# Optimization experiments

Measured on AMD Instinct MI355X. Metric: run time of the kernel, lower is better.

The kernel has to match this reference:

```python
import jax, jax.numpy as jnp
import numpy as np


def lstm_cell(x, h, c, Wih, Whh, bih, bhh):
    # PyTorch LSTMCell: gates ordered [i, f, g, o]
    gates = x @ Wih.T + h @ Whh.T + bih + bhh
    i, f, g, o = jnp.split(gates, 4, axis=-1)
    i = jax.nn.sigmoid(i)
    f = jax.nn.sigmoid(f)
    g = jnp.tanh(g)
    o = jax.nn.sigmoid(o)
    c_new = f * c + i * g
    h_new = o * jnp.tanh(c_new)
    return h_new, c_new


def setup_inputs() -> dict:
    key = jax.random.key(0)
    ks = jax.random.split(key, 16)
    B, T_ENC, T_CENT = 131072, 20, 100
    s32 = 1.0 / np.sqrt(32.0)
    s64 = 1.0 / np.sqrt(64.0)
    s96 = 1.0 / np.sqrt(96.0)
    f32 = jnp.float32
    return {
        "input_traj": jax.random.normal(ks[0], (B, T_ENC, 2), dtype=f32),
        "centerlines": jax.random.normal(ks[1], (B, T_CENT, 2), dtype=f32),
        "Wih_c": jax.random.normal(ks[2], (128, 2), dtype=f32) * s32,
        "Whh_c": jax.random.normal(ks[3], (128, 32), dtype=f32) * s32,
        "bih_c": jax.random.normal(ks[4], (128,), dtype=f32) * s32,
        "bhh_c": jax.random.normal(ks[5], (128,), dtype=f32) * s32,
        "Wih_e": jax.random.normal(ks[6], (256, 2), dtype=f32) * s64,
        "Whh_e": jax.random.normal(ks[7], (256, 64), dtype=f32) * s64,
        "bih_e": jax.random.normal(ks[8], (256,), dtype=f32) * s64,
        "bhh_e": jax.random.normal(ks[9], (256,), dtype=f32) * s64,
        "Wih_d": jax.random.normal(ks[10], (384, 96), dtype=f32) * s96,
        "Whh_d": jax.random.normal(ks[11], (384, 96), dtype=f32) * s96,
        "bih_d": jax.random.normal(ks[12], (384,), dtype=f32) * s96,
        "bhh_d": jax.random.normal(ks[13], (384,), dtype=f32) * s96,
        "W_emb": jax.random.normal(ks[14], (2, 96), dtype=f32) * s96,
        "b_emb": jax.random.normal(ks[15], (2,), dtype=f32) * s96,
    }


def reference(input_traj, centerlines, Wih_c, Whh_c, bih_c, bhh_c,
              Wih_e, Whh_e, bih_e, bhh_e, Wih_d, Whh_d, bih_d, bhh_d,
              W_emb, b_emb):
    B = input_traj.shape[0]
    DEC_STEPS = 30

    # --- centerline embedding LSTM (hidden 32) over max_len steps ---
    def cent_step(carry, x_t):
        h, c = carry
        h, c = lstm_cell(x_t, h, c, Wih_c, Whh_c, bih_c, bhh_c)
        return (h, c), None

    cent_init = (jnp.zeros((B, 32), input_traj.dtype), jnp.zeros((B, 32), input_traj.dtype))
    (cent_h, cent_c), _ = jax.lax.scan(cent_step, cent_init, jnp.swapaxes(centerlines, 0, 1))

    # --- encoder LSTM (hidden 64) over 20 steps ---
    def enc_step(carry, x_t):
        h, c = carry
        h, c = lstm_cell(x_t, h, c, Wih_e, Whh_e, bih_e, bhh_e)
        return (h, c), None

    enc_init = (jnp.zeros((B, 64), input_traj.dtype), jnp.zeros((B, 64), input_traj.dtype))
    (enc_h, enc_c), _ = jax.lax.scan(enc_step, enc_init, jnp.swapaxes(input_traj, 0, 1))

    # --- concat to 96-d state, decode 30 steps feeding h back as input ---
    h0 = jnp.concatenate([enc_h, cent_h], axis=1)  # [B, 96]
    c0 = jnp.concatenate([enc_c, cent_c], axis=1)

    def dec_step(carry, _):
        h, c = carry
        h, c = lstm_cell(h, h, c, Wih_d, Whh_d, bih_d, bhh_d)
        pos = h @ W_emb.T + b_emb  # [B, 2]
        return (h, c), pos

    (_, _), outs = jax.lax.scan(dec_step, (h0, c0), None, length=DEC_STEPS)
    pred_traj = jnp.swapaxes(outs, 0, 1)  # [B, 30, 2]
    return pred_traj
```

## Files before the change

kernel.cpp:

```cpp
#include <hip/hip_runtime.h>


#define B_TOTAL 131072
#define TB 48
#define NBLK ((B_TOTAL + TB - 1) / TB)

typedef __attribute__((ext_vector_type(8))) short bf16x8;
typedef __attribute__((ext_vector_type(4))) float f32x4;

#define MFMA16(a, b, c) __builtin_amdgcn_mfma_f32_16x16x32_bf16((a), (b), (c), 0, 0, 0)

#ifndef __has_builtin
#define __has_builtin(x) 0
#endif
#if __has_builtin(__builtin_amdgcn_exp2f)
#define EXP2(x) __builtin_amdgcn_exp2f(x)
#else
#define EXP2(x) exp2f(x)
#endif
#if __has_builtin(__builtin_amdgcn_rcpf)
#define RCPF(x) __builtin_amdgcn_rcpf(x)
#else
#define RCPF(x) (1.0f / (x))
#endif

#define L2E 1.44269504088896340736f
#define NEG2L2E (-2.88539008177792681472f)

#define OFF_WD_HI 0
#define OFF_WD_LO 36864
#define OFF_WE_HI 73728
#define OFF_WE_LO 98304
#define OFF_WC_HI 122880
#define OFF_WC_LO 131072
#define OFF_WM_HI 139264
#define OFF_WM_LO 140800
#define OFF_BIAS  142336

__device__ __forceinline__ void split2(float f, unsigned short& hi, unsigned short& lo)
{
  unsigned int u = __float_as_uint(f);
  hi = (unsigned short)(u >> 16);
  float r = f - __uint_as_float(u & 0xFFFF0000u);
  lo = (unsigned short)(__float_as_uint(r) >> 16);
}

__device__ __forceinline__ bf16x8 zero8()
{
  bf16x8 z;
#pragma unroll
  for (int e = 0; e < 8; ++e) z[e] = 0;
  return z;
}

__device__ __forceinline__ f32x4 splat4(float v)
{
  f32x4 a; a[0] = v; a[1] = v; a[2] = v; a[3] = v; return a;
}

__device__ __forceinline__ void load_x2(const float* __restrict__ base, long s, int stridef,
                                        int t, bool active, bf16x8& xhi, bf16x8& xlo)
{
  xhi = zero8(); xlo = zero8();
  if (active) {
    const float* p = base + s * (long)stridef + t * 2;
    float x0 = p[0], x1 = p[1];
    unsigned short h0, l0, h1, l1;
    split2(x0, h0, l0); split2(x1, h1, l1);
    xhi[0] = (short)h0; xhi[1] = (short)h1;
    xlo[0] = (short)l0; xlo[1] = (short)l1;
  }
}

__global__ void prep_weights(
    const float* __restrict__ Wih_c, const float* __restrict__ Whh_c,
    const float* __restrict__ bih_c, const float* __restrict__ bhh_c,
    const float* __restrict__ Wih_e, const float* __restrict__ Whh_e,
    const float* __restrict__ bih_e, const float* __restrict__ bhh_e,
    const float* __restrict__ Wih_d, const float* __restrict__ Whh_d,
    const float* __restrict__ bih_d, const float* __restrict__ bhh_d,
    const float* __restrict__ W_emb, const float* __restrict__ b_emb,
    unsigned short* __restrict__ wsu)
{
  int idx = blockIdx.x * 256 + threadIdx.x;
  float* wsf = (float*)(wsu + OFF_BIAS);
  unsigned short h, l;
  if (idx < 384 * 96) {
    int j = idx / 96;
    float s = (j >= 192 && j < 288) ? 2.0f * L2E : L2E;
    float w = (Wih_d[idx] + Whh_d[idx]) * s;
    split2(w, h, l);
    wsu[OFF_WD_HI + idx] = h; wsu[OFF_WD_LO + idx] = l;
  }
  if (idx < 256 * 96) {
    int j = idx / 96, k = idx - j * 96;
    float s = (j >= 128 && j < 192) ? 2.0f * L2E : L2E;
    float w = 0.0f;
    if (k < 64) w = Whh_e[j * 64 + k] * s;
    else if (k < 66) w = Wih_e[j * 2 + (k - 64)] * s;
    split2(w, h, l);
    wsu[OFF_WE_HI + idx] = h; wsu[OFF_WE_LO + idx] = l;
  }
  if (idx < 128 * 64) {
    int j = idx / 64, k = idx - j * 64;
    float s = (j >= 64 && j < 96) ? 2.0f * L2E : L2E;
    float w = 0.0f;
    if (k < 32) w = Whh_c[j * 32 + k] * s;
    else if (k < 34) w = Wih_c[j * 2 + (k - 32)] * s;
    split2(w, h, l);
    wsu[OFF_WC_HI + idx] = h; wsu[OFF_WC_LO + idx] = l;
  }
  if (idx < 16 * 96) {
    int n = idx / 96, k = idx - n * 96;
    float w = (n < 2) ? W_emb[n * 96 + k] : 0.0f;
    split2(w, h, l);
    wsu[OFF_WM_HI + idx] = h; wsu[OFF_WM_LO + idx] = l;
  }
  if (idx < 384) {
    float s = (idx >= 192 && idx < 288) ? 2.0f * L2E : L2E;
    wsf[idx] = (bih_d[idx] + bhh_d[idx]) * s;
  }
  if (idx < 256) {
    float s = (idx >= 128 && idx < 192) ? 2.0f * L2E : L2E;
    wsf[384 + idx] = (bih_e[idx] + bhh_e[idx]) * s;
  }
  if (idx < 128) {
    float s = (idx >= 64 && idx < 96) ? 2.0f * L2E : L2E;
    wsf[640 + idx] = (bih_c[idx] + bhh_c[idx]) * s;
  }
  if (idx < 2) wsf[768 + idx] = b_emb[idx];
}

__global__ __launch_bounds__(384, 2) void lstm_fused(
    const float* __restrict__ traj,
    const float* __restrict__ ctr,
    const unsigned short* __restrict__ wsu,
    float* __restrict__ out)
{
  const int tid = threadIdx.x;
  const int wid = tid >> 6;
  const int lane = tid & 63;
  const int lr = lane & 15;
  const int lg = lane >> 4;
  const int blk = blockIdx.x;

  const float* bias_d = (const float*)(wsu + OFF_BIAS);
  const float* bias_e = bias_d + 384;
  const float* bias_c = bias_d + 640;
  const float* bias_m = bias_d + 768;

  __shared__ __align__(16) unsigned short sh_hi[TB * 104];
  __shared__ __align__(16) unsigned short sh_lo[TB * 104];
  __shared__ __align__(16) unsigned short sBlo[384 * 104];
  __shared__ float sc[TB * 97];

  {
    unsigned int* p0 = (unsigned int*)sh_hi;
    unsigned int* p1 = (unsigned int*)sh_lo;
    for (int i = tid; i < TB * 104 / 2; i += 384) { p0[i] = 0u; p1[i] = 0u; }
  }
  __syncthreads();

  {
    const int ut = wid & 1;
    const int rg = wid >> 1;
    const int ucol = ut * 16 + lr;
    bf16x8 Bh_hi[4], Bh_lo[4], Bx_hi[4], Bx_lo[4];
    float bias[4];
#pragma unroll
    for (int g = 0; g < 4; ++g) {
      int j = g * 32 + ucol;
      Bh_hi[g] = *(const bf16x8*)(wsu + OFF_WC_HI + j * 64 + lg * 8);
      Bh_lo[g] = *(const bf16x8*)(wsu + OFF_WC_LO + j * 64 + lg * 8);
      Bx_hi[g] = *(const bf16x8*)(wsu + OFF_WC_HI + j * 64 + 32 + lg * 8);
      Bx_lo[g] = *(const bf16x8*)(wsu + OFF_WC_LO + j * 64 + 32 + lg * 8);
      bias[g] = bias_c[j];
    }
    float cr[4];
#pragma unroll
    for (int q = 0; q < 4; ++q) cr[q] = 0.0f;
    long srow = (long)blk * TB + rg * 16 + lr;
    if (srow > B_TOTAL - 1) srow = B_TOTAL - 1;
    bf16x8 Ah_hi = *(const bf16x8*)&sh_hi[(rg * 16 + lr) * 104 + 64 + lg * 8];
    bf16x8 Ah_lo = *(const bf16x8*)&sh_lo[(rg * 16 + lr) * 104 + 64 + lg * 8];
    bf16x8 Ax_hi, Ax_lo;
    load_x2(ctr, srow, 200, 0, lg == 0, Ax_hi, Ax_lo);
    for (int t = 0; t < 100; ++t) {
      f32x4 acc[4];
#pragma unroll
      for (int g = 0; g < 4; ++g) {
        f32x4 a = splat4(bias[g]);
        a = MFMA16(Ah_hi, Bh_hi[g], a);
        a = MFMA16(Ah_lo, Bh_hi[g], a);
        a = MFMA16(Ah_hi, Bh_lo[g], a);
        a = MFMA16(Ax_hi, Bx_hi[g], a);
        a = MFMA16(Ax_lo, Bx_hi[g], a);
        a = MFMA16(Ax_hi, Bx_lo[g], a);
        acc[g] = a;
      }
      __syncthreads();
#pragma unroll
      for (int q = 0; q < 4; ++q) {
        float ig = acc[0][q], fg = acc[1][q], gg = acc[2][q], og = acc[3][q];
        float si = RCPF(1.0f + EXP2(-ig));
        float sf = RCPF(1.0f + EXP2(-fg));
        float so = RCPF(1.0f + EXP2(-og));
        float tg = 2.0f * RCPF(1.0f + EXP2(-gg)) - 1.0f;
        float cn = sf * cr[q] + si * tg;
        cr[q] = cn;
        float tc = 2.0f * RCPF(1.0f + EXP2(cn * NEG2L2E)) - 1.0f;
        float hv = so * tc;
        unsigned short hh, hl;
        split2(hv, hh, hl);
        int r = rg * 16 + lg * 4 + q;
        sh_hi[r * 104 + 64 + ucol] = hh;
        sh_lo[r * 104 + 64 + ucol] = hl;
      }
      __syncthreads();
      Ah_hi = *(const bf16x8*)&sh_hi[(rg * 16 + lr) * 104 + 64 + lg * 8];
      Ah_lo = *(const bf16x8*)&sh_lo[(rg * 16 + lr) * 104 + 64 + lg * 8];
      int tn = t < 99 ? t + 1 : 99;
      load_x2(ctr, srow, 200, tn, lg == 0, Ax_hi, Ax_lo);
    }
#pragma unroll
    for (int q = 0; q < 4; ++q)
      sc[(rg * 16 + lg * 4 + q) * 97 + 64 + ucol] = cr[q];
  }
  __syncthreads();

  {
    for (int cid = tid; cid < 256 * 12; cid += 384) {
      int r = cid / 12, ch = cid - r * 12;
      *(bf16x8*)&sBlo[r * 104 + ch * 8] = *(const bf16x8*)(wsu + OFF_WE_LO + r * 96 + ch * 8);
    }
    const bool act = (wid < 4);
    const int ut = wid;
    const int ucol = ut * 16 + lr;
    bf16x8 Bh_hi[4][2], Bx_hi[4];
    float bias[4];
    float cr[3][4];
    long srow[3];
    if (act) {
#pragma unroll
      for (int g = 0; g < 4; ++g) {
        int j = g * 64 + ucol;
#pragma unroll
        for (int kb = 0; kb < 2; ++kb)
          Bh_hi[g][kb] = *(const bf16x8*)(wsu + OFF_WE_HI + j * 96 + kb * 32 + lg * 8);
        Bx_hi[g] = *(const bf16x8*)(wsu + OFF_WE_HI + j * 96 + 64 + lg * 8);
        bias[g] = bias_e[j];
      }
#pragma unroll
      for (int rt = 0; rt < 3; ++rt) {
#pragma unroll
        for (int q = 0; q < 4; ++q) cr[rt][q] = 0.0f;
        long s = (long)blk * TB + rt * 16 + lr;
        srow[rt] = s > B_TOTAL - 1 ? B_TOTAL - 1 : s;
      }
    }
    __syncthreads();
    bf16x8 Ah_hi[3][2], Ax_hi[3], Ax_lo[3];
    if (act) {
#pragma unroll
      for (int rt = 0; rt < 3; ++rt) {
#pragma unroll
        for (int kb = 0; kb < 2; ++kb)
          Ah_hi[rt][kb] = *(const bf16x8*)&sh_hi[(rt * 16 + lr) * 104 + kb * 32 + lg * 8];
        load_x2(traj, srow[rt], 40, 0, lg == 0, Ax_hi[rt], Ax_lo[rt]);
      }
    }
    for (int t = 0; t < 20; ++t) {
      f32x4 acc[3][4];
      if (act) {
#pragma unroll
        for (int rt = 0; rt < 3; ++rt)
#pragma unroll
          for (int g = 0; g < 4; ++g) acc[rt][g] = splat4(bias[g]);
#pragma unroll
        for (int kb = 0; kb < 2; ++kb) {
          bf16x8 alo[3];
#pragma unroll
          for (int rt = 0; rt < 3; ++rt)
            alo[rt] = *(const bf16x8*)&sh_lo[(rt * 16 + lr) * 104 + kb * 32 + lg * 8];
#pragma unroll
          for (int g = 0; g < 4; ++g) {
            bf16x8 blo = *(const bf16x8*)&sBlo[(g * 64 + ucol) * 104 + kb * 32 + lg * 8];
#pragma unroll
            for (int rt = 0; rt < 3; ++rt) {
              acc[rt][g] = MFMA16(Ah_hi[rt][kb], Bh_hi[g][kb], acc[rt][g]);
              acc[rt][g] = MFMA16(alo[rt], Bh_hi[g][kb], acc[rt][g]);
              acc[rt][g] = MFMA16(Ah_hi[rt][kb], blo, acc[rt][g]);
            }
          }
        }
#pragma unroll
        for (int g = 0; g < 4; ++g) {
          bf16x8 blox = *(const bf16x8*)&sBlo[(g * 64 + ucol) * 104 + 64 + lg * 8];
#pragma unroll
          for (int rt = 0; rt < 3; ++rt) {
            acc[rt][g] = MFMA16(Ax_hi[rt], Bx_hi[g], acc[rt][g]);
            acc[rt][g] = MFMA16(Ax_lo[rt], Bx_hi[g], acc[rt][g]);
            acc[rt][g] = MFMA16(Ax_hi[rt], blox, acc[rt][g]);
          }
        }
      }
      __syncthreads();
      if (act) {
#pragma unroll
        for (int rt = 0; rt < 3; ++rt) {
#pragma unroll
          for (int q = 0; q < 4; ++q) {
            float ig = acc[rt][0][q], fg = acc[rt][1][q], gg = acc[rt][2][q], og = acc[rt][3][q];
            float si = RCPF(1.0f + EXP2(-ig));
            float sf = RCPF(1.0f + EXP2(-fg));
            float so = RCPF(1.0f + EXP2(-og));
            float tg = 2.0f * RCPF(1.0f + EXP2(-gg)) - 1.0f;
            float cn = sf * cr[rt][q] + si * tg;
            cr[rt][q] = cn;
            float tc = 2.0f * RCPF(1.0f + EXP2(cn * NEG2L2E)) - 1.0f;
            float hv = so * tc;
            unsigned short hh, hl;
            split2(hv, hh, hl);
            int r = rt * 16 + lg * 4 + q;
            sh_hi[r * 104 + ucol] = hh;
            sh_lo[r * 104 + ucol] = hl;
          }
        }
      }
      __syncthreads();
      if (act) {
#pragma unroll
        for (int rt = 0; rt < 3; ++rt) {
#pragma unroll
          for (int kb = 0; kb < 2; ++kb)
            Ah_hi[rt][kb] = *(const bf16x8*)&sh_hi[(rt * 16 + lr) * 104 + kb * 32 + lg * 8];
          int tn = t < 19 ? t + 1 : 19;
          load_x2(traj, srow[rt], 40, tn, lg == 0, Ax_hi[rt], Ax_lo[rt]);
        }
      }
    }
    if (act) {
#pragma unroll
      for (int rt = 0; rt < 3; ++rt)
#pragma unroll
        for (int q = 0; q < 4; ++q)
          sc[(rt * 16 + lg * 4 + q) * 97 + ucol] = cr[rt][q];
    }
  }
  __syncthreads();

  {
    for (int cid = tid; cid < 384 * 12; cid += 384) {
      int r = cid / 12, ch = cid - r * 12;
      *(bf16x8*)&sBlo[r * 104 + ch * 8] = *(const bf16x8*)(wsu + OFF_WD_LO + r * 96 + ch * 8);
    }
    const int ut = wid;
    const int ucol = ut * 16 + lr;
    bf16x8 Bh_hi[4][3], Bm_hi[3], Bm_lo[3];
    float bias[4];
    float cr[3][4];
#pragma unroll
    for (int g = 0; g < 4; ++g) {
      int j = g * 96 + ucol;
#pragma unroll
      for (int kb = 0; kb < 3; ++kb)
        Bh_hi[g][kb] = *(const bf16x8*)(wsu + OFF_WD_HI + j * 96 + kb * 32 + lg * 8);
      bias[g] = bias_d[j];
    }
#pragma unroll
    for (int kb = 0; kb < 3; ++kb) {
      Bm_hi[kb] = *(const bf16x8*)(wsu + OFF_WM_HI + lr * 96 + kb * 32 + lg * 8);
      Bm_lo[kb] = *(const bf16x8*)(wsu + OFF_WM_LO + lr * 96 + kb * 32 + lg * 8);
    }
    float pbias = (lr < 2) ? bias_m[lr] : 0.0f;
#pragma unroll
    for (int rt = 0; rt < 3; ++rt)
#pragma unroll
      for (int q = 0; q < 4; ++q)
        cr[rt][q] = sc[(rt * 16 + lg * 4 + q) * 97 + ucol];
    __syncthreads();
    bf16x8 Ah_hi[3][3];
#pragma unroll
    for (int rt = 0; rt < 3; ++rt)
#pragma unroll
      for (int kb = 0; kb < 3; ++kb)
        Ah_hi[rt][kb] = *(const bf16x8*)&sh_hi[(rt * 16 + lr) * 104 + kb * 32 + lg * 8];
    for (int t = 0; t < 30; ++t) {
      f32x4 acc[3][4];
#pragma unroll
      for (int rt = 0; rt < 3; ++rt)
#pragma unroll
        for (int g = 0; g < 4; ++g) acc[rt][g] = splat4(bias[g]);
#pragma unroll
      for (int kb = 0; kb < 3; ++kb) {
        bf16x8 alo[3];
#pragma unroll
        for (int rt = 0; rt < 3; ++rt)
          alo[rt] = *(const bf16x8*)&sh_lo[(rt * 16 + lr) * 104 + kb * 32 + lg * 8];
#pragma unroll
        for (int g = 0; g < 4; ++g) {
          bf16x8 blo = *(const bf16x8*)&sBlo[(g * 96 + ucol) * 104 + kb * 32 + lg * 8];
#pragma unroll
          for (int rt = 0; rt < 3; ++rt) {
            acc[rt][g] = MFMA16(Ah_hi[rt][kb], Bh_hi[g][kb], acc[rt][g]);
            acc[rt][g] = MFMA16(alo[rt], Bh_hi[g][kb], acc[rt][g]);
            acc[rt][g] = MFMA16(Ah_hi[rt][kb], blo, acc[rt][g]);
          }
        }
      }
      __syncthreads();
#pragma unroll
      for (int rt = 0; rt < 3; ++rt) {
#pragma unroll
        for (int q = 0; q < 4; ++q) {
          float ig = acc[rt][0][q], fg = acc[rt][1][q], gg = acc[rt][2][q], og = acc[rt][3][q];
          float si = RCPF(1.0f + EXP2(-ig));
          float sf = RCPF(1.0f + EXP2(-fg));
          float so = RCPF(1.0f + EXP2(-og));
          float tg = 2.0f * RCPF(1.0f + EXP2(-gg)) - 1.0f;
          float cn = sf * cr[rt][q] + si * tg;
          cr[rt][q] = cn;
          float tc = 2.0f * RCPF(1.0f + EXP2(cn * NEG2L2E)) - 1.0f;
          float hv = so * tc;
          unsigned short hh, hl;
          split2(hv, hh, hl);
          int r = rt * 16 + lg * 4 + q;
          sh_hi[r * 104 + ucol] = hh;
          sh_lo[r * 104 + ucol] = hl;
        }
      }
      __syncthreads();
#pragma unroll
      for (int rt = 0; rt < 3; ++rt)
#pragma unroll
        for (int kb = 0; kb < 3; ++kb)
          Ah_hi[rt][kb] = *(const bf16x8*)&sh_hi[(rt * 16 + lr) * 104 + kb * 32 + lg * 8];
      if (wid < 3) {
        f32x4 ap = splat4(pbias);
#pragma unroll
        for (int kb = 0; kb < 3; ++kb) {
          bf16x8 ahi = *(const bf16x8*)&sh_hi[(wid * 16 + lr) * 104 + kb * 32 + lg * 8];
          bf16x8 alo = *(const bf16x8*)&sh_lo[(wid * 16 + lr) * 104 + kb * 32 + lg * 8];
          ap = MFMA16(ahi, Bm_hi[kb], ap);
          ap = MFMA16(alo, Bm_hi[kb], ap);
          ap = MFMA16(ahi, Bm_lo[kb], ap);
        }
        if (lr < 2) {
#pragma unroll
          for (int q = 0; q < 4; ++q) {
            long s = (long)blk * TB + wid * 16 + lg * 4 + q;
            if (s < B_TOTAL) out[s * 60 + t * 2 + lr] = ap[q];
          }
        }
      }
    }
  }
}

extern "C" void kernel_launch(void* const* d_in, const int* in_sizes, int n_in,
                              void* d_out, int out_size, void* d_ws, size_t ws_size,
                              hipStream_t stream)
{
  if (ws_size < 287752) return;
  const float* traj = (const float*)d_in[0];
  const float* ctr  = (const float*)d_in[1];
  prep_weights<<<144, 256, 0, stream>>>(
      (const float*)d_in[2],  (const float*)d_in[3],  (const float*)d_in[4],  (const float*)d_in[5],
      (const float*)d_in[6],  (const float*)d_in[7],  (const float*)d_in[8],  (const float*)d_in[9],
      (const float*)d_in[10], (const float*)d_in[11], (const float*)d_in[12], (const float*)d_in[13],
      (const float*)d_in[14], (const float*)d_in[15],
      (unsigned short*)d_ws);
  lstm_fused<<<NBLK, 384, 0, stream>>>(traj, ctr, (const unsigned short*)d_ws, (float*)d_out);
}
```

Before: 3.005 ms.

## Double-buffer hidden state, drop LDS weight staging, and raise occupancy to three blocks

The hidden-state LDS buffers become ping-pong buffers, so each recurrent step needs one barrier instead of two. The low-half weight tiles are no longer staged in LDS (about 80 KB); they are read from global memory inside the step loops. The output-projection weights are now loaded per step instead of held in registers. Cutting LDS and register use makes room for `__launch_bounds__(384, 3)` and more resident blocks per CU, which should better hide the latency of the serial recurrence. The cost is repeated global/L1 loads of weight fragments on every time step.

New measurement: 4.190 ms. 39.4% more time.

```diff
diff --git a/kernel.cpp b/kernel.cpp
--- a/kernel.cpp
+++ b/kernel.cpp
@@ -131,7 +131,7 @@
   if (idx < 2) wsf[768 + idx] = b_emb[idx];
 }
 
-__global__ __launch_bounds__(384, 2) void lstm_fused(
+__global__ __launch_bounds__(384, 3) void lstm_fused(
     const float* __restrict__ traj,
     const float* __restrict__ ctr,
     const unsigned short* __restrict__ wsu,
@@ -149,15 +149,14 @@
   const float* bias_c = bias_d + 640;
   const float* bias_m = bias_d + 768;
 
-  __shared__ __align__(16) unsigned short sh_hi[TB * 104];
-  __shared__ __align__(16) unsigned short sh_lo[TB * 104];
-  __shared__ __align__(16) unsigned short sBlo[384 * 104];
+  __shared__ __align__(16) unsigned short sh_hi[2][TB * 104];
+  __shared__ __align__(16) unsigned short sh_lo[2][TB * 104];
   __shared__ float sc[TB * 97];
 
   {
     unsigned int* p0 = (unsigned int*)sh_hi;
     unsigned int* p1 = (unsigned int*)sh_lo;
-    for (int i = tid; i < TB * 104 / 2; i += 384) { p0[i] = 0u; p1[i] = 0u; }
+    for (int i = tid; i < 2 * TB * 104 / 2; i += 384) { p0[i] = 0u; p1[i] = 0u; }
   }
   __syncthreads();
 
@@ -181,11 +180,12 @@
     for (int q = 0; q < 4; ++q) cr[q] = 0.0f;
     long srow = (long)blk * TB + rg * 16 + lr;
     if (srow > B_TOTAL - 1) srow = B_TOTAL - 1;
-    bf16x8 Ah_hi = *(const bf16x8*)&sh_hi[(rg * 16 + lr) * 104 + 64 + lg * 8];
-    bf16x8 Ah_lo = *(const bf16x8*)&sh_lo[(rg * 16 + lr) * 104 + 64 + lg * 8];
     bf16x8 Ax_hi, Ax_lo;
     load_x2(ctr, srow, 200, 0, lg == 0, Ax_hi, Ax_lo);
     for (int t = 0; t < 100; ++t) {
+      const int cur = t & 1;
+      bf16x8 Ah_hi = *(const bf16x8*)&sh_hi[cur][(rg * 16 + lr) * 104 + 64 + lg * 8];
+      bf16x8 Ah_lo = *(const bf16x8*)&sh_lo[cur][(rg * 16 + lr) * 104 + 64 + lg * 8];
       f32x4 acc[4];
 #pragma unroll
       for (int g = 0; g < 4; ++g) {
@@ -198,7 +198,6 @@
         a = MFMA16(Ax_hi, Bx_lo[g], a);
         acc[g] = a;
       }
-      __syncthreads();
 #pragma unroll
       for (int q = 0; q < 4; ++q) {
         float ig = acc[0][q], fg = acc[1][q], gg = acc[2][q], og = acc[3][q];
@@ -213,14 +212,12 @@
         unsigned short hh, hl;
         split2(hv, hh, hl);
         int r = rg * 16 + lg * 4 + q;
-        sh_hi[r * 104 + 64 + ucol] = hh;
-        sh_lo[r * 104 + 64 + ucol] = hl;
-      }
-      __syncthreads();
-      Ah_hi = *(const bf16x8*)&sh_hi[(rg * 16 + lr) * 104 + 64 + lg * 8];
-      Ah_lo = *(const bf16x8*)&sh_lo[(rg * 16 + lr) * 104 + 64 + lg * 8];
+        sh_hi[cur ^ 1][r * 104 + 64 + ucol] = hh;
+        sh_lo[cur ^ 1][r * 104 + 64 + ucol] = hl;
+      }
       int tn = t < 99 ? t + 1 : 99;
       load_x2(ctr, srow, 200, tn, lg == 0, Ax_hi, Ax_lo);
+      __syncthreads();
     }
 #pragma unroll
     for (int q = 0; q < 4; ++q)
@@ -229,10 +226,6 @@
   __syncthreads();
 
   {
-    for (int cid = tid; cid < 256 * 12; cid += 384) {
-      int r = cid / 12, ch = cid - r * 12;
-      *(bf16x8*)&sBlo[r * 104 + ch * 8] = *(const bf16x8*)(wsu + OFF_WE_LO + r * 96 + ch * 8);
-    }
     const bool act = (wid < 4);
     const int ut = wid;
     const int ucol = ut * 16 + lr;
@@ -258,18 +251,14 @@
         srow[rt] = s > B_TOTAL - 1 ? B_TOTAL - 1 : s;
       }
     }
-    __syncthreads();
-    bf16x8 Ah_hi[3][2], Ax_hi[3], Ax_lo[3];
+    bf16x8 Ax_hi[3], Ax_lo[3];
     if (act) {
 #pragma unroll
-      for (int rt = 0; rt < 3; ++rt) {
-#pragma unroll
-        for (int kb = 0; kb < 2; ++kb)
-          Ah_hi[rt][kb] = *(const bf16x8*)&sh_hi[(rt * 16 + lr) * 104 + kb * 32 + lg * 8];
+      for (int rt = 0; rt < 3; ++rt)
         load_x2(traj, srow[rt], 40, 0, lg == 0, Ax_hi[rt], Ax_lo[rt]);
-      }
     }
     for (int t = 0; t < 20; ++t) {
+      const int cur = t & 1;
       f32x4 acc[3][4];
       if (act) {
 #pragma unroll
@@ -278,24 +267,26 @@
           for (int g = 0; g < 4; ++g) acc[rt][g] = splat4(bias[g]);
 #pragma unroll
         for (int kb = 0; kb < 2; ++kb) {
-          bf16x8 alo[3];
-#pragma unroll
-          for (int rt = 0; rt < 3; ++rt)
-            alo[rt] = *(const bf16x8*)&sh_lo[(rt * 16 + lr) * 104 + kb * 32 + lg * 8];
+          bf16x8 ahi[3], alo[3];
+#pragma unroll
+          for (int rt = 0; rt < 3; ++rt) {
+            ahi[rt] = *(const bf16x8*)&sh_hi[cur][(rt * 16 + lr) * 104 + kb * 32 + lg * 8];
+            alo[rt] = *(const bf16x8*)&sh_lo[cur][(rt * 16 + lr) * 104 + kb * 32 + lg * 8];
+          }
 #pragma unroll
           for (int g = 0; g < 4; ++g) {
-            bf16x8 blo = *(const bf16x8*)&sBlo[(g * 64 + ucol) * 104 + kb * 32 + lg * 8];
+            bf16x8 blo = *(const bf16x8*)(wsu + OFF_WE_LO + (g * 64 + ucol) * 96 + kb * 32 + lg * 8);
 #pragma unroll
             for (int rt = 0; rt < 3; ++rt) {
-              acc[rt][g] = MFMA16(Ah_hi[rt][kb], Bh_hi[g][kb], acc[rt][g]);
+              acc[rt][g] = MFMA16(ahi[rt], Bh_hi[g][kb], acc[rt][g]);
               acc[rt][g] = MFMA16(alo[rt], Bh_hi[g][kb], acc[rt][g]);
-              acc[rt][g] = MFMA16(Ah_hi[rt][kb], blo, acc[rt][g]);
+              acc[rt][g] = MFMA16(ahi[rt], blo, acc[rt][g]);
             }
           }
         }
 #pragma unroll
         for (int g = 0; g < 4; ++g) {
-          bf16x8 blox = *(const bf16x8*)&sBlo[(g * 64 + ucol) * 104 + 64 + lg * 8];
+          bf16x8 blox = *(const bf16x8*)(wsu + OFF_WE_LO + (g * 64 + ucol) * 96 + 64 + lg * 8);
 #pragma unroll
           for (int rt = 0; rt < 3; ++rt) {
             acc[rt][g] = MFMA16(Ax_hi[rt], Bx_hi[g], acc[rt][g]);
@@ -303,9 +294,6 @@
             acc[rt][g] = MFMA16(Ax_hi[rt], blox, acc[rt][g]);
           }
         }
-      }
-      __syncthreads();
-      if (act) {
 #pragma unroll
         for (int rt = 0; rt < 3; ++rt) {
 #pragma unroll
@@ -322,22 +310,16 @@
             unsigned short hh, hl;
             split2(hv, hh, hl);
             int r = rt * 16 + lg * 4 + q;
-            sh_hi[r * 104 + ucol] = hh;
-            sh_lo[r * 104 + ucol] = hl;
-          }
-        }
+            sh_hi[cur ^ 1][r * 104 + ucol] = hh;
+            sh_lo[cur ^ 1][r * 104 + ucol] = hl;
+          }
+        }
+        int tn = t < 19 ? t + 1 : 19;
+#pragma unroll
+        for (int rt = 0; rt < 3; ++rt)
+          load_x2(traj, srow[rt], 40, tn, lg == 0, Ax_hi[rt], Ax_lo[rt]);
       }
       __syncthreads();
-      if (act) {
-#pragma unroll
-        for (int rt = 0; rt < 3; ++rt) {
-#pragma unroll
-          for (int kb = 0; kb < 2; ++kb)
-            Ah_hi[rt][kb] = *(const bf16x8*)&sh_hi[(rt * 16 + lr) * 104 + kb * 32 + lg * 8];
-          int tn = t < 19 ? t + 1 : 19;
-          load_x2(traj, srow[rt], 40, tn, lg == 0, Ax_hi[rt], Ax_lo[rt]);
-        }
-      }
     }
     if (act) {
 #pragma unroll
@@ -350,13 +332,9 @@
   __syncthreads();
 
   {
-    for (int cid = tid; cid < 384 * 12; cid += 384) {
-      int r = cid / 12, ch = cid - r * 12;
-      *(bf16x8*)&sBlo[r * 104 + ch * 8] = *(const bf16x8*)(wsu + OFF_WD_LO + r * 96 + ch * 8);
-    }
     const int ut = wid;
     const int ucol = ut * 16 + lr;
-    bf16x8 Bh_hi[4][3], Bm_hi[3], Bm_lo[3];
+    bf16x8 Bh_hi[4][3];
     float bias[4];
     float cr[3][4];
 #pragma unroll
@@ -367,25 +345,14 @@
         Bh_hi[g][kb] = *(const bf16x8*)(wsu + OFF_WD_HI + j * 96 + kb * 32 + lg * 8);
       bias[g] = bias_d[j];
     }
-#pragma unroll
-    for (int kb = 0; kb < 3; ++kb) {
-      Bm_hi[kb] = *(const bf16x8*)(wsu + OFF_WM_HI + lr * 96 + kb * 32 + lg * 8);
-      Bm_lo[kb] = *(const bf16x8*)(wsu + OFF_WM_LO + lr * 96 + kb * 32 + lg * 8);
-    }
     float pbias = (lr < 2) ? bias_m[lr] : 0.0f;
 #pragma unroll
     for (int rt = 0; rt < 3; ++rt)
 #pragma unroll
       for (int q = 0; q < 4; ++q)
         cr[rt][q] = sc[(rt * 16 + lg * 4 + q) * 97 + ucol];
-    __syncthreads();
-    bf16x8 Ah_hi[3][3];
-#pragma unroll
-    for (int rt = 0; rt < 3; ++rt)
-#pragma unroll
-      for (int kb = 0; kb < 3; ++kb)
-        Ah_hi[rt][kb] = *(const bf16x8*)&sh_hi[(rt * 16 + lr) * 104 + kb * 32 + lg * 8];
     for (int t = 0; t < 30; ++t) {
+      const int cur = t & 1;
       f32x4 acc[3][4];
 #pragma unroll
       for (int rt = 0; rt < 3; ++rt)
@@ -393,22 +360,23 @@
         for (int g = 0; g < 4; ++g) acc[rt][g] = splat4(bias[g]);
 #pragma unroll
       for (int kb = 0; kb < 3; ++kb) {
-        bf16x8 alo[3];
-#pragma unroll
-        for (int rt = 0; rt < 3; ++rt)
-          alo[rt] = *(const bf16x8*)&sh_lo[(rt * 16 + lr) * 104 + kb * 32 + lg * 8];
+        bf16x8 ahi[3], alo[3];
+#pragma unroll
+        for (int rt = 0; rt < 3; ++rt) {
+          ahi[rt] = *(const bf16x8*)&sh_hi[cur][(rt * 16 + lr) * 104 + kb * 32 + lg * 8];
+          alo[rt] = *(const bf16x8*)&sh_lo[cur][(rt * 16 + lr) * 104 + kb * 32 + lg * 8];
+        }
 #pragma unroll
         for (int g = 0; g < 4; ++g) {
-          bf16x8 blo = *(const bf16x8*)&sBlo[(g * 96 + ucol) * 104 + kb * 32 + lg * 8];
+          bf16x8 blo = *(const bf16x8*)(wsu + OFF_WD_LO + (g * 96 + ucol) * 96 + kb * 32 + lg * 8);
 #pragma unroll
           for (int rt = 0; rt < 3; ++rt) {
-            acc[rt][g] = MFMA16(Ah_hi[rt][kb], Bh_hi[g][kb], acc[rt][g]);
+            acc[rt][g] = MFMA16(ahi[rt], Bh_hi[g][kb], acc[rt][g]);
             acc[rt][g] = MFMA16(alo[rt], Bh_hi[g][kb], acc[rt][g]);
-            acc[rt][g] = MFMA16(Ah_hi[rt][kb], blo, acc[rt][g]);
-          }
-        }
-      }
-      __syncthreads();
+            acc[rt][g] = MFMA16(ahi[rt], blo, acc[rt][g]);
+          }
+        }
+      }
 #pragma unroll
       for (int rt = 0; rt < 3; ++rt) {
 #pragma unroll
@@ -425,25 +393,22 @@
           unsigned short hh, hl;
           split2(hv, hh, hl);
           int r = rt * 16 + lg * 4 + q;
-          sh_hi[r * 104 + ucol] = hh;
-          sh_lo[r * 104 + ucol] = hl;
+          sh_hi[cur ^ 1][r * 104 + ucol] = hh;
+          sh_lo[cur ^ 1][r * 104 + ucol] = hl;
         }
       }
       __syncthreads();
-#pragma unroll
-      for (int rt = 0; rt < 3; ++rt)
-#pragma unroll
-        for (int kb = 0; kb < 3; ++kb)
-          Ah_hi[rt][kb] = *(const bf16x8*)&sh_hi[(rt * 16 + lr) * 104 + kb * 32 + lg * 8];
       if (wid < 3) {
         f32x4 ap = splat4(pbias);
 #pragma unroll
         for (int kb = 0; kb < 3; ++kb) {
-          bf16x8 ahi = *(const bf16x8*)&sh_hi[(wid * 16 + lr) * 104 + kb * 32 + lg * 8];
-          bf16x8 alo = *(const bf16x8*)&sh_lo[(wid * 16 + lr) * 104 + kb * 32 + lg * 8];
-          ap = MFMA16(ahi, Bm_hi[kb], ap);
-          ap = MFMA16(alo, Bm_hi[kb], ap);
-          ap = MFMA16(ahi, Bm_lo[kb], ap);
+          bf16x8 ahi = *(const bf16x8*)&sh_hi[cur ^ 1][(wid * 16 + lr) * 104 + kb * 32 + lg * 8];
+          bf16x8 alo = *(const bf16x8*)&sh_lo[cur ^ 1][(wid * 16 + lr) * 104 + kb * 32 + lg * 8];
+          bf16x8 bmh = *(const bf16x8*)(wsu + OFF_WM_HI + lr * 96 + kb * 32 + lg * 8);
+          bf16x8 bml = *(const bf16x8*)(wsu + OFF_WM_LO + lr * 96 + kb * 32 + lg * 8);
+          ap = MFMA16(ahi, bmh, ap);
+          ap = MFMA16(alo, bmh, ap);
+          ap = MFMA16(ahi, bml, ap);
         }
         if (lr < 2) {
 #pragma unroll
```
